# Optimization experiments

Measured on AMD Instinct MI355X. Metric: run time of the kernel, lower is better.

The kernel has to match this reference:

```python
import jax, jax.numpy as jnp
import numpy as np

B, T, D = 64, 4096, 100   # batch, tokens, token_dim == code_dim
K = 4                     # discrete_size: codebook entries
BETA = 0.25               # commitment loss weight


def setup_inputs() -> dict:
    key = jax.random.key(0)
    k_x, k_w, k_b, k_c = jax.random.split(key, 4)
    x = jax.random.normal(k_x, (B, T, D), dtype=jnp.float32)
    W1 = jax.random.normal(k_w, (D, D), dtype=jnp.float32) * (1.0 / np.sqrt(D))
    b1 = jax.random.normal(k_b, (D,), dtype=jnp.float32) * 0.01
    codebook = jax.random.normal(k_c, (K, D), dtype=jnp.float32)
    return {"x": x, "W1": W1, "b1": b1, "codebook": codebook, "quantize": 1}


def reference(x, W1, b1, codebook, quantize):
    # Linear1: Linear(100,100) + ReLU (torch Linear: x @ W.T + b)
    h = jax.nn.relu(jnp.einsum("btd,ed->bte", x, W1) + b1)  # [B,T,D]
    if not quantize:
        return (h, 0, 0, 0)
    # quantizer.compress: VQ-style cdist/argmin/straight-through/loss
    flat = h.reshape(-1, D)  # [N,D]
    d2 = (jnp.sum(flat * flat, axis=-1, keepdims=True)
          - 2.0 * flat @ codebook.T
          + jnp.sum(codebook * codebook, axis=-1))
    idx = jnp.argmin(d2, axis=-1)          # [N] nearest code indices
    q = codebook[idx]                       # [N,D] gathered codes
    sg = jax.lax.stop_gradient
    # codebook loss + commitment loss
    vq_loss = (jnp.mean((sg(flat) - q) ** 2)
               + BETA * jnp.mean((flat - sg(q)) ** 2))
    # straight-through quantized output
    aux = (flat + sg(q - flat)).reshape(B, T, D)
    payload = idx.reshape(B, T)
    return (h, payload, aux, vq_loss)
```

## Files before the change

kernel.cpp:

```cpp
#include <hip/hip_runtime.h>

#define D_DIM   100
#define K_CODES 4
#define RPB     64
#define TPB     256
#define PITCH   65
#define N_ROWS  262144
#define KP      128
#define NP      128
#define TAU     0.25
#define GRID_GEMM 1024
#define NTILES  4

typedef __attribute__((ext_vector_type(8))) __bf16 bf16x8;
typedef __attribute__((ext_vector_type(4))) float  f32x4;

__device__ __forceinline__ unsigned short f2bf_rne(float f) {
    unsigned int u = __builtin_bit_cast(unsigned int, f);
    unsigned int r = u + 0x7fffu + ((u >> 16) & 1u);
    return (unsigned short)(r >> 16);
}
__device__ __forceinline__ float bf2f(unsigned short b) {
    unsigned int u = ((unsigned int)b) << 16;
    return __builtin_bit_cast(float, u);
}

__device__ __forceinline__ void load_lds16(const float* g, float* s) {
    __builtin_amdgcn_global_load_lds(
        (const __attribute__((address_space(1))) unsigned int*)g,
        (__attribute__((address_space(3))) unsigned int*)s, 16, 0, 0);
}

__device__ __forceinline__ void stage_x(const float* xg, float* s, int wave, int lane) {
    #pragma unroll
    for (int it = 0; it < 6; ++it) {
        int cbase = it * 256 + wave * 64;
        load_lds16(xg + (size_t)(cbase + lane) * 4, s + cbase * 4);
    }
    if (wave == 0) load_lds16(xg + (size_t)(1536 + lane) * 4, s + 1536 * 4);
}

__global__ __launch_bounds__(256) void split_w_kernel(
    const float* __restrict__ W1,
    unsigned short* __restrict__ Whi, unsigned short* __restrict__ Wlo)
{
    int i = blockIdx.x * 256 + threadIdx.x;
    if (i >= NP * KP) return;
    int n = i / KP, k = i % KP;
    float w = (n < D_DIM && k < D_DIM) ? W1[n * D_DIM + k] : 0.0f;
    unsigned short hb = f2bf_rne(w);
    float lo = w - bf2f(hb);
    Whi[i] = hb;
    Wlo[i] = f2bf_rne(lo);
}

__global__ __launch_bounds__(TPB, 4) void gemm_relu_mfma(
    const float* __restrict__ x,
    const unsigned short* __restrict__ Whi, const unsigned short* __restrict__ Wlo,
    const float* __restrict__ b1, float* __restrict__ out_h)
{
    __shared__ __align__(16) float buf0[6500];
    __shared__ __align__(16) float buf1[6500];
    const int tid  = threadIdx.x;
    const int lane = tid & 63;
    const int wave = tid >> 6;

    const int bcol0 = wave * 32;
    const int bn  = lane & 15;
    const int bk  = (lane >> 4) * 8;
    bf16x8 bh[2][4], bl[2][4];
    #pragma unroll
    for (int ct = 0; ct < 2; ++ct) {
        int n = bcol0 + ct * 16 + bn;
        #pragma unroll
        for (int kt = 0; kt < 4; ++kt) {
            int off = n * KP + kt * 32 + bk;
            bh[ct][kt] = *reinterpret_cast<const bf16x8*>(Whi + off);
            bl[ct][kt] = *reinterpret_cast<const bf16x8*>(Wlo + off);
        }
    }
    float bias[2];
    #pragma unroll
    for (int ct = 0; ct < 2; ++ct) {
        int n = bcol0 + ct * 16 + bn;
        bias[ct] = (n < D_DIM) ? b1[n] : 0.0f;
    }

    if (tid < 32) { buf0[6400 + tid] = 0.0f; buf1[6400 + tid] = 0.0f; }

    stage_x(x + (size_t)blockIdx.x * RPB * D_DIM, buf0, wave, lane);

    const int am = lane & 15;
    const int ak = (lane >> 4) * 8;

    for (int it = 0; it < NTILES; ++it) {
        const int tile = blockIdx.x + it * GRID_GEMM;
        const int rowBase = tile * RPB;
        float* cur = (it & 1) ? buf1 : buf0;
        float* nxt = (it & 1) ? buf0 : buf1;

        __syncthreads();

        if (it + 1 < NTILES)
            stage_x(x + (size_t)(blockIdx.x + (it + 1) * GRID_GEMM) * RPB * D_DIM,
                    nxt, wave, lane);

        f32x4 acc[4][2];
        #pragma unroll
        for (int rt = 0; rt < 4; ++rt) {
            acc[rt][0] = (f32x4){0.f, 0.f, 0.f, 0.f};
            acc[rt][1] = (f32x4){0.f, 0.f, 0.f, 0.f};
        }
        #pragma unroll
        for (int rt = 0; rt < 4; ++rt) {
            const int rbase = (rt * 16 + am) * D_DIM;
            #pragma unroll
            for (int kt = 0; kt < 4; ++kt) {
                const float* p = cur + rbase + kt * 32 + ak;
                f32x4 f0 = *reinterpret_cast<const f32x4*>(p);
                f32x4 f1 = *reinterpret_cast<const f32x4*>(p + 4);
                bf16x8 ah, al;
                #pragma unroll
                for (int i = 0; i < 4; ++i) {
                    __bf16 h0 = (__bf16)f0[i];
                    ah[i] = h0;
                    al[i] = (__bf16)(f0[i] - (float)h0);
                    __bf16 h1 = (__bf16)f1[i];
                    ah[4 + i] = h1;
                    al[4 + i] = (__bf16)(f1[i] - (float)h1);
                }
                acc[rt][0] = __builtin_amdgcn_mfma_f32_16x16x32_bf16(ah, bl[0][kt], acc[rt][0], 0, 0, 0);
                acc[rt][0] = __builtin_amdgcn_mfma_f32_16x16x32_bf16(al, bh[0][kt], acc[rt][0], 0, 0, 0);
                acc[rt][0] = __builtin_amdgcn_mfma_f32_16x16x32_bf16(ah, bh[0][kt], acc[rt][0], 0, 0, 0);
                acc[rt][1] = __builtin_amdgcn_mfma_f32_16x16x32_bf16(ah, bl[1][kt], acc[rt][1], 0, 0, 0);
                acc[rt][1] = __builtin_amdgcn_mfma_f32_16x16x32_bf16(al, bh[1][kt], acc[rt][1], 0, 0, 0);
                acc[rt][1] = __builtin_amdgcn_mfma_f32_16x16x32_bf16(ah, bh[1][kt], acc[rt][1], 0, 0, 0);
            }
        }
        __syncthreads();

        #pragma unroll
        for (int rt = 0; rt < 4; ++rt) {
            int rb = rt * 16 + (lane >> 4) * 4;
            #pragma unroll
            for (int ct = 0; ct < 2; ++ct) {
                int n = bcol0 + ct * 16 + bn;
                if (n < D_DIM) {
                    #pragma unroll
                    for (int i = 0; i < 4; ++i)
                        cur[n * PITCH + rb + i] = fmaxf(acc[rt][ct][i] + bias[ct], 0.0f);
                }
            }
        }
        __syncthreads();

        float* hg = out_h + (size_t)rowBase * D_DIM;
        for (int v = tid; v < RPB * 25; v += TPB) {
            int r = v / 25;
            int d = (v % 25) * 4;
            reinterpret_cast<float4*>(hg)[v] = make_float4(
                cur[d * PITCH + r], cur[(d + 1) * PITCH + r],
                cur[(d + 2) * PITCH + r], cur[(d + 3) * PITCH + r]);
        }
    }
}

__global__ __launch_bounds__(TPB) void vq_kernel(
    const float* __restrict__ h, const float* __restrict__ x,
    const float* __restrict__ W1, const float* __restrict__ b1,
    const float* __restrict__ cb, const int* __restrict__ qflag,
    float* __restrict__ out_pay, float* __restrict__ out_aux,
    double* __restrict__ partials)
{
    __shared__ float  tile[D_DIM][PITCH];
    __shared__ double d2s[K_CODES][RPB];
    __shared__ int    idxs[RPB];
    __shared__ unsigned long long flagmask;
    const int tid  = threadIdx.x;
    const int lane = tid & 63;
    const int wave = tid >> 6;
    const int blk  = blockIdx.x;
    const int rowBase = blk * RPB;
    const int qz = *qflag;

    if (qz) {
        const float* hgc = h + (size_t)rowBase * D_DIM;
        for (int v = tid; v < (RPB * D_DIM) / 4; v += TPB) {
            float4 val = reinterpret_cast<const float4*>(hgc)[v];
            int r = v / 25;
            int d = (v % 25) * 4;
            tile[d + 0][r] = val.x; tile[d + 1][r] = val.y;
            tile[d + 2][r] = val.z; tile[d + 3][r] = val.w;
        }
        __syncthreads();
        {
            const int k = __builtin_amdgcn_readfirstlane(wave & 3);
            const float* crow = cb + k * D_DIM;
            double s = 0.0;
            #pragma unroll
            for (int d = 0; d < D_DIM; ++d) {
                double dh = (double)tile[d][lane] - (double)crow[d];
                s = fma(dh, dh, s);
            }
            d2s[k][lane] = s;
        }
        __syncthreads();

        if (wave == 0) {
            double best = d2s[0][lane], second = 1e300;
            int bi = 0;
            #pragma unroll
            for (int k = 1; k < K_CODES; ++k) {
                double v = d2s[k][lane];
                if (v < best) { second = best; best = v; bi = k; }
                else if (v < second) { second = v; }
            }
            idxs[lane] = bi;
            unsigned long long m = __ballot((second - best) < TAU);
            if (lane == 0) flagmask = m;
        }
        __syncthreads();

        {
            unsigned long long m = flagmask;
            int i = 0;
            while (m) {
                int r = __ffsll((long long)m) - 1;
                m &= m - 1;
                if ((i & 3) == wave) {
                    const int e1 = lane;
                    const int e2 = 64 + lane;
                    const bool has2 = (e2 < D_DIM);
                    float z1 = b1[e1];
                    float z2 = has2 ? b1[e2] : 0.0f;
                    const float* xr  = x + (size_t)(rowBase + r) * D_DIM;
                    const float* w1r = W1 + e1 * D_DIM;
                    const float* w2r = W1 + (has2 ? e2 : 0) * D_DIM;
                    #pragma unroll
                    for (int d4 = 0; d4 < 25; ++d4) {
                        float4 xv = reinterpret_cast<const float4*>(xr)[d4];
                        float4 wa = reinterpret_cast<const float4*>(w1r)[d4];
                        z1 = fmaf(xv.x, wa.x, z1); z1 = fmaf(xv.y, wa.y, z1);
                        z1 = fmaf(xv.z, wa.z, z1); z1 = fmaf(xv.w, wa.w, z1);
                        float4 wb = reinterpret_cast<const float4*>(w2r)[d4];
                        z2 = fmaf(xv.x, wb.x, z2); z2 = fmaf(xv.y, wb.y, z2);
                        z2 = fmaf(xv.z, wb.z, z2); z2 = fmaf(xv.w, wb.w, z2);
                    }
                    float h1 = fmaxf(z1, 0.0f);
                    float h2 = fmaxf(z2, 0.0f);
                    double dk[K_CODES];
                    #pragma unroll
                    for (int k = 0; k < K_CODES; ++k) {
                        double p;
                        {
                            double dh = (double)h1 - (double)cb[k * D_DIM + e1];
                            p = dh * dh;
                        }
                        if (has2) {
                            double dh = (double)h2 - (double)cb[k * D_DIM + e2];
                            p = fma(dh, dh, p);
                        }
                        for (int off = 32; off > 0; off >>= 1)
                            p += __shfl_down(p, off);
                        dk[k] = p;
                    }
                    if (lane == 0) {
                        double best = dk[0];
                        int bi = 0;
                        #pragma unroll
                        for (int k = 1; k < K_CODES; ++k)
                            if (dk[k] < best) { best = dk[k]; bi = k; }
                        idxs[r] = bi;
                    }
                }
                ++i;
            }
        }
        __syncthreads();

        if (wave == 0) {
            int bi = idxs[lane];
            out_pay[rowBase + lane] = (float)bi;
            double d2min = d2s[bi][lane];
            for (int off = 32; off > 0; off >>= 1)
                d2min += __shfl_down(d2min, off);
            if (lane == 0) partials[blk] = d2min;
        }

        float* ag = out_aux + (size_t)rowBase * D_DIM;
        for (int v = tid; v < (RPB * D_DIM) / 4; v += TPB) {
            int r = v / 25;
            int d = (v % 25) * 4;
            int bi = idxs[r];
            reinterpret_cast<float4*>(ag)[v] =
                reinterpret_cast<const float4*>(cb + bi * D_DIM + d)[0];
        }
    } else {
        if (wave == 0) {
            out_pay[rowBase + lane] = 0.0f;
            if (lane == 0) partials[blk] = 0.0;
        }
        float* ag = out_aux + (size_t)rowBase * D_DIM;
        for (int v = tid; v < (RPB * D_DIM) / 4; v += TPB)
            reinterpret_cast<float4*>(ag)[v] = make_float4(0, 0, 0, 0);
    }
}

__global__ __launch_bounds__(256) void vq_final_kernel(
    const double* __restrict__ partials, int n, float* __restrict__ loss_out)
{
    __shared__ double sm[256];
    int tid = threadIdx.x;
    double s = 0.0;
    for (int i = tid; i < n; i += 256) s += partials[i];
    sm[tid] = s;
    __syncthreads();
    for (int off = 128; off > 0; off >>= 1) {
        if (tid < off) sm[tid] += sm[tid + off];
        __syncthreads();
    }
    if (tid == 0) {
        double mse = sm[0] / ((double)N_ROWS * (double)D_DIM);
        loss_out[0] = (float)(1.25 * mse);
    }
}

extern "C" void kernel_launch(void* const* d_in, const int* in_sizes, int n_in,
                              void* d_out, int out_size, void* d_ws, size_t ws_size,
                              hipStream_t stream) {
    const float* x  = (const float*)d_in[0];
    const float* W1 = (const float*)d_in[1];
    const float* b1 = (const float*)d_in[2];
    const float* cb = (const float*)d_in[3];
    const int* qflag = (const int*)d_in[4];

    float* out = (float*)d_out;
    const int NR = in_sizes[0] / D_DIM;
    const int nblocks = NR / RPB;

    float* out_h    = out;
    float* out_pay  = out + (size_t)NR * D_DIM;
    float* out_aux  = out_pay + NR;
    float* out_loss = out_aux + (size_t)NR * D_DIM;

    double* partials = (double*)d_ws;
    const size_t w_off = (size_t)nblocks * sizeof(double);
    unsigned short* Whi = (unsigned short*)((char*)d_ws + w_off);
    unsigned short* Wlo = Whi + NP * KP;

    split_w_kernel<<<(NP * KP) / 256, 256, 0, stream>>>(W1, Whi, Wlo);
    gemm_relu_mfma<<<GRID_GEMM, TPB, 0, stream>>>(x, Whi, Wlo, b1, out_h);
    vq_kernel<<<nblocks, TPB, 0, stream>>>(out_h, x, W1, b1, cb, qflag,
                                           out_pay, out_aux, partials);
    vq_final_kernel<<<1, 256, 0, stream>>>(partials, nblocks, out_loss);
}
```

Measured before the change: 117.6 us.

## Make VQ kernel wave-independent with fp32 distances and a wider exact-recheck margin

The VQ kernel is restructured so each wave owns 64 rows and each lane computes its row's four codebook distances in fp32, reading h directly from global memory. This removes the LDS transpose, the fp64 distance loop and the block-level barriers. Rows whose best and second-best distances are close are recomputed exactly from x and W1 inside the same wave, with the margin raised to absorb fp32 error. In exchange, per-lane row reads are strided, more rows may take the slow exact path, and the loss partials are now built from fp32 distances.

```diff
diff --git a/kernel.cpp b/kernel.cpp
--- a/kernel.cpp
+++ b/kernel.cpp
@@ -8,7 +8,7 @@
 #define N_ROWS  262144
 #define KP      128
 #define NP      128
-#define TAU     0.25
+#define TAU     2.0f
 #define GRID_GEMM 1024
 #define NTILES  4
 
@@ -24,13 +24,11 @@
     unsigned int u = ((unsigned int)b) << 16;
     return __builtin_bit_cast(float, u);
 }
-
 __device__ __forceinline__ void load_lds16(const float* g, float* s) {
     __builtin_amdgcn_global_load_lds(
         (const __attribute__((address_space(1))) unsigned int*)g,
         (__attribute__((address_space(3))) unsigned int*)s, 16, 0, 0);
 }
-
 __device__ __forceinline__ void stage_x(const float* xg, float* s, int wave, int lane) {
     #pragma unroll
     for (int it = 0; it < 6; ++it) {
@@ -38,6 +36,55 @@
         load_lds16(xg + (size_t)(cbase + lane) * 4, s + cbase * 4);
     }
     if (wave == 0) load_lds16(xg + (size_t)(1536 + lane) * 4, s + 1536 * 4);
+}
+
+__device__ __forceinline__ int exact_row_argmin(
+    const float* __restrict__ x, const float* __restrict__ W1,
+    const float* __restrict__ b1, const float* __restrict__ cb,
+    int gr, int lane)
+{
+    const int e1 = lane;
+    const int e2 = 64 + lane;
+    const bool has2 = (e2 < D_DIM);
+    float z1 = b1[e1];
+    float z2 = has2 ? b1[e2] : 0.0f;
+    const float* xr  = x + (size_t)gr * D_DIM;
+    const float* w1r = W1 + e1 * D_DIM;
+    const float* w2r = W1 + (has2 ? e2 : 0) * D_DIM;
+    #pragma unroll
+    for (int d4 = 0; d4 < 25; ++d4) {
+        float4 xv = reinterpret_cast<const float4*>(xr)[d4];
+        float4 wa = reinterpret_cast<const float4*>(w1r)[d4];
+        z1 = fmaf(xv.x, wa.x, z1); z1 = fmaf(xv.y, wa.y, z1);
+        z1 = fmaf(xv.z, wa.z, z1); z1 = fmaf(xv.w, wa.w, z1);
+        float4 wb = reinterpret_cast<const float4*>(w2r)[d4];
+        z2 = fmaf(xv.x, wb.x, z2); z2 = fmaf(xv.y, wb.y, z2);
+        z2 = fmaf(xv.z, wb.z, z2); z2 = fmaf(xv.w, wb.w, z2);
+    }
+    float h1 = fmaxf(z1, 0.0f);
+    float h2 = fmaxf(z2, 0.0f);
+    double dk[K_CODES];
+    #pragma unroll
+    for (int k = 0; k < K_CODES; ++k) {
+        double p;
+        {
+            double dh = (double)h1 - (double)cb[k * D_DIM + e1];
+            p = dh * dh;
+        }
+        if (has2) {
+            double dh = (double)h2 - (double)cb[k * D_DIM + e2];
+            p = fma(dh, dh, p);
+        }
+        for (int off = 32; off > 0; off >>= 1)
+            p += __shfl_down(p, off);
+        dk[k] = p;
+    }
+    int bi_ex = 0;
+    double best = dk[0];
+    #pragma unroll
+    for (int k = 1; k < K_CODES; ++k)
+        if (dk[k] < best) { best = dk[k]; bi_ex = k; }
+    return __shfl(bi_ex, 0);
 }
 
 __global__ __launch_bounds__(256) void split_w_kernel(
@@ -85,9 +132,7 @@
         int n = bcol0 + ct * 16 + bn;
         bias[ct] = (n < D_DIM) ? b1[n] : 0.0f;
     }
-
     if (tid < 32) { buf0[6400 + tid] = 0.0f; buf1[6400 + tid] = 0.0f; }
-
     stage_x(x + (size_t)blockIdx.x * RPB * D_DIM, buf0, wave, lane);
 
     const int am = lane & 15;
@@ -100,7 +145,6 @@
         float* nxt = (it & 1) ? buf0 : buf1;
 
         __syncthreads();
-
         if (it + 1 < NTILES)
             stage_x(x + (size_t)(blockIdx.x + (it + 1) * GRID_GEMM) * RPB * D_DIM,
                     nxt, wave, lane);
@@ -165,144 +209,77 @@
     }
 }
 
-__global__ __launch_bounds__(TPB) void vq_kernel(
+__global__ __launch_bounds__(TPB, 4) void vq_kernel(
     const float* __restrict__ h, const float* __restrict__ x,
     const float* __restrict__ W1, const float* __restrict__ b1,
     const float* __restrict__ cb, const int* __restrict__ qflag,
     float* __restrict__ out_pay, float* __restrict__ out_aux,
     double* __restrict__ partials)
 {
-    __shared__ float  tile[D_DIM][PITCH];
-    __shared__ double d2s[K_CODES][RPB];
-    __shared__ int    idxs[RPB];
-    __shared__ unsigned long long flagmask;
-    const int tid  = threadIdx.x;
-    const int lane = tid & 63;
-    const int wave = tid >> 6;
-    const int blk  = blockIdx.x;
-    const int rowBase = blk * RPB;
+    const int lane = threadIdx.x & 63;
+    const int wave = threadIdx.x >> 6;
+    const int wg   = blockIdx.x * 4 + wave;
+    const int rowBase = wg * 64;
     const int qz = *qflag;
 
     if (qz) {
-        const float* hgc = h + (size_t)rowBase * D_DIM;
-        for (int v = tid; v < (RPB * D_DIM) / 4; v += TPB) {
-            float4 val = reinterpret_cast<const float4*>(hgc)[v];
+        const float* hr = h + (size_t)(rowBase + lane) * D_DIM;
+        float s[K_CODES] = {0.f, 0.f, 0.f, 0.f};
+        #pragma unroll
+        for (int c = 0; c < 25; ++c) {
+            f32x4 hv = *reinterpret_cast<const f32x4*>(hr + c * 4);
+            #pragma unroll
+            for (int k = 0; k < K_CODES; ++k) {
+                f32x4 cv = *reinterpret_cast<const f32x4*>(cb + k * D_DIM + c * 4);
+                #pragma unroll
+                for (int i = 0; i < 4; ++i) {
+                    float e = hv[i] - cv[i];
+                    s[k] = fmaf(e, e, s[k]);
+                }
+            }
+        }
+        float best = s[0], second = 3.4e38f;
+        int bi = 0;
+        #pragma unroll
+        for (int k = 1; k < K_CODES; ++k) {
+            float v = s[k];
+            if (v < best) { second = best; best = v; bi = k; }
+            else if (v < second) { second = v; }
+        }
+        const bool flg = (second - best) < TAU;
+
+        unsigned long long m = __ballot(flg);
+        while (m) {
+            int r = __ffsll((long long)m) - 1;
+            m &= m - 1;
+            int bx = exact_row_argmin(x, W1, b1, cb, rowBase + r, lane);
+            if (lane == r) bi = bx;
+        }
+
+        out_pay[rowBase + lane] = (float)bi;
+
+        double la = (double)s[bi];
+        for (int off = 32; off > 0; off >>= 1)
+            la += __shfl_down(la, off);
+        if (lane == 0) partials[wg] = la;
+
+        float* ag = out_aux + (size_t)rowBase * D_DIM;
+        #pragma unroll
+        for (int it = 0; it < 25; ++it) {
+            int v = it * 64 + lane;
             int r = v / 25;
             int d = (v % 25) * 4;
-            tile[d + 0][r] = val.x; tile[d + 1][r] = val.y;
-            tile[d + 2][r] = val.z; tile[d + 3][r] = val.w;
-        }
-        __syncthreads();
-        {
-            const int k = __builtin_amdgcn_readfirstlane(wave & 3);
-            const float* crow = cb + k * D_DIM;
-            double s = 0.0;
-            #pragma unroll
-            for (int d = 0; d < D_DIM; ++d) {
-                double dh = (double)tile[d][lane] - (double)crow[d];
-                s = fma(dh, dh, s);
-            }
-            d2s[k][lane] = s;
-        }
-        __syncthreads();
-
-        if (wave == 0) {
-            double best = d2s[0][lane], second = 1e300;
-            int bi = 0;
-            #pragma unroll
-            for (int k = 1; k < K_CODES; ++k) {
-                double v = d2s[k][lane];
-                if (v < best) { second = best; best = v; bi = k; }
-                else if (v < second) { second = v; }
-            }
-            idxs[lane] = bi;
-            unsigned long long m = __ballot((second - best) < TAU);
-            if (lane == 0) flagmask = m;
-        }
-        __syncthreads();
-
-        {
-            unsigned long long m = flagmask;
-            int i = 0;
-            while (m) {
-                int r = __ffsll((long long)m) - 1;
-                m &= m - 1;
-                if ((i & 3) == wave) {
-                    const int e1 = lane;
-                    const int e2 = 64 + lane;
-                    const bool has2 = (e2 < D_DIM);
-                    float z1 = b1[e1];
-                    float z2 = has2 ? b1[e2] : 0.0f;
-                    const float* xr  = x + (size_t)(rowBase + r) * D_DIM;
-                    const float* w1r = W1 + e1 * D_DIM;
-                    const float* w2r = W1 + (has2 ? e2 : 0) * D_DIM;
-                    #pragma unroll
-                    for (int d4 = 0; d4 < 25; ++d4) {
-                        float4 xv = reinterpret_cast<const float4*>(xr)[d4];
-                        float4 wa = reinterpret_cast<const float4*>(w1r)[d4];
-                        z1 = fmaf(xv.x, wa.x, z1); z1 = fmaf(xv.y, wa.y, z1);
-                        z1 = fmaf(xv.z, wa.z, z1); z1 = fmaf(xv.w, wa.w, z1);
-                        float4 wb = reinterpret_cast<const float4*>(w2r)[d4];
-                        z2 = fmaf(xv.x, wb.x, z2); z2 = fmaf(xv.y, wb.y, z2);
-                        z2 = fmaf(xv.z, wb.z, z2); z2 = fmaf(xv.w, wb.w, z2);
-                    }
-                    float h1 = fmaxf(z1, 0.0f);
-                    float h2 = fmaxf(z2, 0.0f);
-                    double dk[K_CODES];
-                    #pragma unroll
-                    for (int k = 0; k < K_CODES; ++k) {
-                        double p;
-                        {
-                            double dh = (double)h1 - (double)cb[k * D_DIM + e1];
-                            p = dh * dh;
-                        }
-                        if (has2) {
-                            double dh = (double)h2 - (double)cb[k * D_DIM + e2];
-                            p = fma(dh, dh, p);
-                        }
-                        for (int off = 32; off > 0; off >>= 1)
-                            p += __shfl_down(p, off);
-                        dk[k] = p;
-                    }
-                    if (lane == 0) {
-                        double best = dk[0];
-                        int bi = 0;
-                        #pragma unroll
-                        for (int k = 1; k < K_CODES; ++k)
-                            if (dk[k] < best) { best = dk[k]; bi = k; }
-                        idxs[r] = bi;
-                    }
-                }
-                ++i;
-            }
-        }
-        __syncthreads();
-
-        if (wave == 0) {
-            int bi = idxs[lane];
-            out_pay[rowBase + lane] = (float)bi;
-            double d2min = d2s[bi][lane];
-            for (int off = 32; off > 0; off >>= 1)
-                d2min += __shfl_down(d2min, off);
-            if (lane == 0) partials[blk] = d2min;
-        }
-
+            int bir = __shfl(bi, r);
+            reinterpret_cast<float4*>(ag)[v] =
+                *reinterpret_cast<const float4*>(cb + bir * D_DIM + d);
+        }
+    } else {
+        out_pay[rowBase + lane] = 0.0f;
+        if (lane == 0) partials[wg] = 0.0;
         float* ag = out_aux + (size_t)rowBase * D_DIM;
-        for (int v = tid; v < (RPB * D_DIM) / 4; v += TPB) {
-            int r = v / 25;
-            int d = (v % 25) * 4;
-            int bi = idxs[r];
-            reinterpret_cast<float4*>(ag)[v] =
-                reinterpret_cast<const float4*>(cb + bi * D_DIM + d)[0];
-        }
-    } else {
-        if (wave == 0) {
-            out_pay[rowBase + lane] = 0.0f;
-            if (lane == 0) partials[blk] = 0.0;
-        }
-        float* ag = out_aux + (size_t)rowBase * D_DIM;
-        for (int v = tid; v < (RPB * D_DIM) / 4; v += TPB)
-            reinterpret_cast<float4*>(ag)[v] = make_float4(0, 0, 0, 0);
+        #pragma unroll
+        for (int it = 0; it < 25; ++it)
+            reinterpret_cast<float4*>(ag)[it * 64 + lane] = make_float4(0, 0, 0, 0);
     }
 }
 
@@ -350,7 +327,7 @@
 
     split_w_kernel<<<(NP * KP) / 256, 256, 0, stream>>>(W1, Whi, Wlo);
     gemm_relu_mfma<<<GRID_GEMM, TPB, 0, stream>>>(x, Whi, Wlo, b1, out_h);
-    vq_kernel<<<nblocks, TPB, 0, stream>>>(out_h, x, W1, b1, cb, qflag,
-                                           out_pay, out_aux, partials);
+    vq_kernel<<<GRID_GEMM, TPB, 0, stream>>>(out_h, x, W1, b1, cb, qflag,
+                                             out_pay, out_aux, partials);
     vq_final_kernel<<<1, 256, 0, stream>>>(partials, nblocks, out_loss);
 }
```

Measured after the change: 339.5 us. 189% more time.
